# Kernel optimization log

Hardware: AMD Instinct MI355X
Metric: run time of the kernel (lower is better)

Reference implementation:

```python
import jax, jax.numpy as jnp
import numpy as np

B, S, I, H, O, L = 32, 512, 1024, 1024, 1024, 3


def setup_inputs() -> dict:
    key = jax.random.key(0)
    ks = jax.random.split(key, 16)
    sw = 1.0 / np.sqrt(H)  # roughly torch Linear init scale
    inp = {
        "x": jax.random.normal(ks[0], (B, S, I), jnp.float32),
        "h0": jax.random.normal(ks[1], (B, L, H), jnp.float32),
        # gate weights stacked over layers; stored (in, out) so y = x @ W
        "Wx":  jax.random.normal(ks[2], (L, I, H), jnp.float32) * sw,
        "Wz":  jax.random.normal(ks[3], (L, H, H), jnp.float32) * sw,
        "bz":  jax.random.normal(ks[4], (L, H), jnp.float32),   # init.normal_ in original
        "Wr":  jax.random.normal(ks[5], (L, I, H), jnp.float32) * sw,
        "Wh":  jax.random.normal(ks[6], (L, H, H), jnp.float32) * sw,
        "br":  jax.random.normal(ks[7], (L, H), jnp.float32),
        "Wg":  jax.random.normal(ks[8], (L, I, H), jnp.float32) * sw,
        "Whg": jax.random.normal(ks[9], (L, H, H), jnp.float32) * sw,
        "bg":  jax.random.normal(ks[10], (L, H), jnp.float32),
        "Wout": jax.random.normal(ks[11], (H, O), jnp.float32) * sw,
        "bout": jax.random.normal(ks[12], (O,), jnp.float32) * sw,
    }
    return inp


def reference(x, h0, Wx, Wz, bz, Wr, Wh, br, Wg, Whg, bg, Wout, bout):
    n_layers = Wx.shape[0]
    # Original quirk: layer_states only ever gains the LAST layer's ht each
    # timestep; state for layer j at step t is layer_states[t + j]. That is a
    # sliding window of length n_layers over [init states, last-layer hts...].
    window0 = jnp.transpose(h0, (1, 0, 2))  # (L, B, H)

    def step(window, xt):  # window: (L,B,H), xt: (B,I)
        inp = xt
        ht = window[-1]
        for j in range(n_layers):
            s = window[j]
            zt = jax.nn.sigmoid(inp @ Wx[j] + s @ Wz[j] + bz[j])
            rt = jax.nn.sigmoid(inp @ Wr[j] + s @ Wh[j] + br[j])
            ht = zt * s + (1.0 - zt) * jnp.tanh(
                inp @ Wg[j] + (rt * s) @ Whg[j] + bg[j])
            inp = ht  # dropout p=0 is identity
        new_window = jnp.concatenate([window[1:], ht[None]], axis=0)
        y = inp @ Wout + bout
        return new_window, (y, ht)

    _, (ys, hts) = jax.lax.scan(step, window0, jnp.transpose(x, (1, 0, 2)))
    layer_output = jnp.transpose(ys, (1, 0, 2))          # (B, S, O)
    hidden_state = jnp.transpose(hts[-n_layers:], (1, 0, 2))  # (B, L, H)
    return layer_output, hidden_state
```

## Files before the change

### kernel.cpp

```cpp
#include <hip/hip_runtime.h>

#define B_ 32
#define S_ 512
#define H_ 1024
#define L_ 3
#define BH (B_*H_)
#define NBLK 512
#define PLANE 32768

typedef __attribute__((ext_vector_type(8))) short short8;
typedef __attribute__((ext_vector_type(4))) float f4;

__device__ __forceinline__ unsigned short f2bf(float f){
  unsigned int u = __float_as_uint(f);
  u += 0x7fffu + ((u >> 16) & 1u);
  return (unsigned short)(u >> 16);
}
__device__ __forceinline__ float sigmoidf_(float x){
  return 1.0f / (1.0f + __expf(-x));
}
__device__ __forceinline__ int afrag_off(int b, int n){
  int mh = b >> 4, row = b & 15;
  int kb = n >> 5, quad = (n >> 3) & 3, j = n & 7;
  return (((mh * 32 + kb) * 64) + quad * 16 + row) * 8 + j;
}

template<bool DC>
__device__ __forceinline__ short8 ldA(const unsigned short* p){
  short8 v;
  if constexpr (DC)
    asm volatile("global_load_dwordx4 %0, %1, off sc1" : "=&v"(v) : "v"(p));
  else
    asm volatile("global_load_dwordx4 %0, %1, off" : "=&v"(v) : "v"(p));
  return v;
}
template<int N>
__device__ __forceinline__ void waitv(){
  asm volatile("s_waitcnt vmcnt(%0)" :: "i"(N));
  __builtin_amdgcn_sched_barrier(0);
}
__device__ __forceinline__ float ldf_dc(const float* p){
  return __hip_atomic_load(p, __ATOMIC_RELAXED, __HIP_MEMORY_SCOPE_AGENT);
}
__device__ __forceinline__ void stf_dc(float* p, float v){
  __hip_atomic_store(p, v, __ATOMIC_RELAXED, __HIP_MEMORY_SCOPE_AGENT);
}
__device__ __forceinline__ void stu16_dc(unsigned short* p, unsigned short v){
  __hip_atomic_store(p, v, __ATOMIC_RELAXED, __HIP_MEMORY_SCOPE_AGENT);
}

__global__ void prep_WA_packed(const float* __restrict__ Wx, const float* __restrict__ Wz,
                               const float* __restrict__ Wr, const float* __restrict__ Wh,
                               unsigned short* __restrict__ WAp){
  int idx = blockIdx.x * blockDim.x + threadIdx.x;
  int lane = idx & 63;
  int kb = (idx >> 6) & 63;
  int tile = idx >> 12;
  int g = tile >> 7, jt = tile & 127;
  int quad = lane >> 4, l15 = lane & 15;
  int n = jt * 16 + l15;
  int k0 = kb * 32 + quad * 8;
  int col = n & 1023;
  const float* W = (k0 < 1024) ? ((n < 1024) ? Wx : Wr) : ((n < 1024) ? Wz : Wh);
  const float* src = W + ((size_t)g * 1024 + (k0 & 1023)) * 1024 + col;
  short8 v;
  #pragma unroll
  for (int j = 0; j < 8; ++j) v[j] = (short)f2bf(src[(size_t)j * 1024]);
  *(short8*)(WAp + (size_t)idx * 8) = v;
}

__global__ void prep_WB_packed(const float* __restrict__ Wg, const float* __restrict__ Whg,
                               unsigned short* __restrict__ WBp){
  int idx = blockIdx.x * blockDim.x + threadIdx.x;
  int lane = idx & 63;
  int kb = (idx >> 6) & 63;
  int tile = idx >> 12;
  int g = tile >> 6, jt = tile & 63;
  int quad = lane >> 4, l15 = lane & 15;
  int n = jt * 16 + l15;
  int k0 = kb * 32 + quad * 8;
  const float* W = (k0 < 1024) ? Wg : Whg;
  const float* src = W + ((size_t)g * 1024 + (k0 & 1023)) * 1024 + n;
  short8 v;
  #pragma unroll
  for (int j = 0; j < 8; ++j) v[j] = (short)f2bf(src[(size_t)j * 1024]);
  *(short8*)(WBp + (size_t)idx * 8) = v;
}

__global__ void prep_Wout_packed(const float* __restrict__ Wout,
                                 unsigned short* __restrict__ WoutP){
  int idx = blockIdx.x * blockDim.x + threadIdx.x;
  int lane = idx & 63;
  int kb = (idx >> 6) & 31;
  int tile = idx >> 11;
  int quad = lane >> 4, l15 = lane & 15;
  int n = tile * 16 + l15;
  int k0 = kb * 32 + quad * 8;
  const float* src = Wout + (size_t)k0 * 1024 + n;
  short8 v;
  #pragma unroll
  for (int j = 0; j < 8; ++j) v[j] = (short)f2bf(src[(size_t)j * 1024]);
  *(short8*)(WoutP + (size_t)idx * 8) = v;
}

__global__ void prep_X_packed(const float* __restrict__ x, unsigned short* __restrict__ Xp){
  size_t idx = (size_t)blockIdx.x * blockDim.x + threadIdx.x;
  int j = (int)(idx & 7);
  int lane = (int)((idx >> 3) & 63);
  int kb = (int)((idx >> 9) & 31);
  int mh = (int)((idx >> 14) & 1);
  int t = (int)(idx >> 15);
  int b = mh * 16 + (lane & 15);
  int i = kb * 32 + (lane >> 4) * 8 + j;
  Xp[idx] = f2bf(x[((size_t)b * S_ + t) * 1024 + i]);
}

__global__ void prep_H0_kernel(const float* __restrict__ h0,
                               unsigned short* __restrict__ HTb, float* __restrict__ HTf,
                               unsigned short* __restrict__ hfinp){
  int idx = blockIdx.x * blockDim.x + threadIdx.x;
  int h = idx & 1023;
  int b = (idx >> 10) & 31;
  int v = idx >> 15;
  float val = h0[((size_t)b * L_ + v) * 1024 + h];
  HTb[idx] = f2bf(val);
  HTf[idx] = val;
  hfinp[(size_t)v * PLANE + afrag_off(b, h)] = f2bf(val);
}

__device__ __forceinline__ void tree_barrier(unsigned* bar, unsigned target){
  __syncthreads();
  if (threadIdx.x == 0){
    unsigned* sub = bar + (blockIdx.x & 7) * 16;
    unsigned* top = bar + 128;
    unsigned* gen = bar + 144;
    unsigned old = __hip_atomic_fetch_add(sub, 1u, __ATOMIC_RELAXED, __HIP_MEMORY_SCOPE_AGENT);
    if (old == target * (NBLK / 8) - 1u){
      unsigned t2 = __hip_atomic_fetch_add(top, 1u, __ATOMIC_RELAXED, __HIP_MEMORY_SCOPE_AGENT);
      if (t2 == target * 8u - 1u)
        __hip_atomic_store(gen, target, __ATOMIC_RELAXED, __HIP_MEMORY_SCOPE_AGENT);
    }
    while (__hip_atomic_load(gen, __ATOMIC_RELAXED, __HIP_MEMORY_SCOPE_AGENT) < target)
      __builtin_amdgcn_s_sleep(1);
  }
  __syncthreads();
}

template<bool DCI>
__device__ __forceinline__ f4 gemm64_lds(const unsigned short* __restrict__ inp,
                                         const unsigned short* __restrict__ st,
                                         const unsigned short* w,
                                         int mh, int lane){
  const unsigned short* pi = inp + mh * 16384 + lane * 8;
  const unsigned short* ps = st  + mh * 16384 + lane * 8;
  short8 ab[4][8];
  #pragma unroll
  for (int b = 0; b < 4; ++b)
    #pragma unroll
    for (int j = 0; j < 8; ++j)
      ab[b][j] = ldA<DCI>(pi + (size_t)(b * 8 + j) * 512);
  f4 acc = {0.f, 0.f, 0.f, 0.f};
  #pragma unroll
  for (int b = 0; b < 4; ++b){
    short8 wv[8];
    #pragma unroll
    for (int j = 0; j < 8; ++j)
      wv[j] = *(const short8*)(w + (size_t)((b * 8 + j) * 64 + lane) * 8);
    waitv<24>();
    #pragma unroll
    for (int j = 0; j < 8; ++j)
      acc = __builtin_amdgcn_mfma_f32_16x16x32_bf16(ab[b][j], wv[j], acc, 0, 0, 0);
    #pragma unroll
    for (int j = 0; j < 8; ++j)
      ab[b][j] = ldA<true>(ps + (size_t)(b * 8 + j) * 512);
  }
  #pragma unroll
  for (int b = 0; b < 4; ++b){
    short8 wv[8];
    #pragma unroll
    for (int j = 0; j < 8; ++j)
      wv[j] = *(const short8*)(w + (size_t)((32 + b * 8 + j) * 64 + lane) * 8);
    if (b == 0) waitv<24>();
    else if (b == 1) waitv<16>();
    else if (b == 2) waitv<8>();
    else waitv<0>();
    #pragma unroll
    for (int j = 0; j < 8; ++j)
      acc = __builtin_amdgcn_mfma_f32_16x16x32_bf16(ab[b][j], wv[j], acc, 0, 0, 0);
  }
  return acc;
}

__device__ __forceinline__ f4 gemm64_gw(const unsigned short* __restrict__ inp,
                                        const unsigned short* __restrict__ st,
                                        const unsigned short* __restrict__ wg,
                                        int mh, int lane){
  const unsigned short* pi = inp + mh * 16384 + lane * 8;
  const unsigned short* ps = st  + mh * 16384 + lane * 8;
  const unsigned short* pw = wg + lane * 8;
  short8 ab[2][8], wb[2][8];
  #pragma unroll
  for (int b = 0; b < 2; ++b){
    #pragma unroll
    for (int j = 0; j < 8; ++j) ab[b][j] = ldA<true>(pi + (size_t)(b * 8 + j) * 512);
    #pragma unroll
    for (int j = 0; j < 8; ++j) wb[b][j] = ldA<false>(pw + (size_t)(b * 8 + j) * 512);
  }
  f4 acc = {0.f, 0.f, 0.f, 0.f};
  #pragma unroll
  for (int b = 0; b < 8; ++b){
    if (b < 7) waitv<16>(); else waitv<0>();
    #pragma unroll
    for (int j = 0; j < 8; ++j)
      acc = __builtin_amdgcn_mfma_f32_16x16x32_bf16(ab[b & 1][j], wb[b & 1][j], acc, 0, 0, 0);
    if (b < 6){
      const int nb = b + 2;
      #pragma unroll
      for (int j = 0; j < 8; ++j){
        if (nb < 4) ab[b & 1][j] = ldA<true>(pi + (size_t)(nb * 8 + j) * 512);
        else        ab[b & 1][j] = ldA<true>(ps + (size_t)((nb - 4) * 8 + j) * 512);
      }
      #pragma unroll
      for (int j = 0; j < 8; ++j)
        wb[b & 1][j] = ldA<false>(pw + (size_t)(nb * 8 + j) * 512);
    }
  }
  return acc;
}

__global__ __launch_bounds__(128) void gru_persist(
    const unsigned short* __restrict__ WAp, const unsigned short* __restrict__ WBp,
    const unsigned short* __restrict__ Xp,
    unsigned short* __restrict__ hL0p, unsigned short* __restrict__ hL1p,
    unsigned short* __restrict__ hfinp,
    unsigned short* __restrict__ HTb, float* __restrict__ HTf,
    float* __restrict__ zbuf, unsigned short* __restrict__ rsp,
    const float* __restrict__ bz, const float* __restrict__ br,
    const float* __restrict__ bg, unsigned* bar)
{
  __shared__ unsigned short ldsw[32768];
  const int blk = blockIdx.x;
  const int lane = threadIdx.x & 63;
  const int mh = threadIdx.x >> 6;
  const int quad = lane >> 4, l15 = lane & 15;

  {
    const unsigned short* src = (blk < 384) ? WAp + (size_t)blk * 32768
                                            : WBp + (size_t)(blk - 384) * 32768;
    for (int i = threadIdx.x; i < 4096; i += 128)
      *(short8*)(ldsw + (size_t)i * 8) = *(const short8*)(src + (size_t)i * 8);
  }
  __syncthreads();

  const int gA = blk >> 7, jtA = blk & 127;
  int gB = -1, jtB = 0;
  const unsigned short* wBg = nullptr;
  if (blk >= 384){ gB = (blk - 384) >> 6; jtB = (blk - 384) & 63; }
  else if (blk >= 320){ gB = 2; jtB = blk - 320; wBg = WBp + (size_t)(128 + (blk - 320)) * 32768; }

  float biasA = 0.f, biasB = 0.f;
  if (blk < 384){
    int n2 = jtA * 16 + l15;
    biasA = (jtA < 64) ? bz[gA * H_ + n2] : br[gA * H_ + n2 - 1024];
  }
  if (gB >= 0) biasB = bg[gB * H_ + jtB * 16 + l15];

  unsigned tgt = 1;
  for (int s = -4; s <= 2 * S_ - 1; ++s){
    int u = ((s & 1) ? (s - 1) : s) / 2;
    int v = u + 2;
    if (!(s & 1)){
      if (blk < 384){
        int t = u + 2 - gA;
        if (t >= 0 && t < S_){
          int tm = t & 3;
          const unsigned short* inp = (gA == 0) ? Xp + (size_t)t * PLANE
                                    : (gA == 1) ? hL0p + (size_t)tm * PLANE
                                                : hL1p + (size_t)tm * PLANE;
          const unsigned short* st = hfinp + (size_t)(v & 7) * PLANE;
          f4 acc = (gA == 0) ? gemm64_lds<false>(inp, st, ldsw, mh, lane)
                             : gemm64_lds<true >(inp, st, ldsw, mh, lane);
          int n2 = jtA * 16 + l15;
          const float* sf = HTf + (size_t)(v & 7) * BH;
          if (jtA < 64){
            float* zb = zbuf + (size_t)(gA * 4 + tm) * BH;
            #pragma unroll
            for (int r = 0; r < 4; ++r){
              int b = mh * 16 + quad * 4 + r;
              stf_dc(zb + b * H_ + n2, sigmoidf_(acc[r] + biasA));
            }
          } else {
            int n = n2 - 1024;
            unsigned short* rp = rsp + (size_t)(gA * 4 + tm) * PLANE;
            #pragma unroll
            for (int r = 0; r < 4; ++r){
              int b = mh * 16 + quad * 4 + r;
              float sv = ldf_dc(sf + b * H_ + n);
              stu16_dc(rp + afrag_off(b, n), f2bf(sigmoidf_(acc[r] + biasA) * sv));
            }
          }
        }
      }
    } else {
      if (gB >= 0){
        int t = u + 2 - gB;
        if (t >= 0 && t < S_){
          int tm = t & 3;
          const unsigned short* inp = (gB == 0) ? Xp + (size_t)t * PLANE
                                    : (gB == 1) ? hL0p + (size_t)tm * PLANE
                                                : hL1p + (size_t)tm * PLANE;
          const unsigned short* rp = rsp + (size_t)(gB * 4 + tm) * PLANE;
          f4 acc;
          if (wBg)          acc = gemm64_gw(inp, rp, wBg, mh, lane);
          else if (gB == 0) acc = gemm64_lds<false>(inp, rp, ldsw, mh, lane);
          else              acc = gemm64_lds<true >(inp, rp, ldsw, mh, lane);
          int n = jtB * 16 + l15;
          const float* sf = HTf + (size_t)(v & 7) * BH;
          const float* zb = zbuf + (size_t)(gB * 4 + tm) * BH;
          #pragma unroll
          for (int r = 0; r < 4; ++r){
            int b = mh * 16 + quad * 4 + r;
            float gg = tanhf(acc[r] + biasB);
            float z = ldf_dc(zb + b * H_ + n);
            float sv = ldf_dc(sf + b * H_ + n);
            float h = z * sv + (1.f - z) * gg;
            unsigned short hb = f2bf(h);
            if (gB == 2){
              stf_dc(HTf + (size_t)((t + 3) & 7) * BH + b * H_ + n, h);
              HTb[(size_t)(t + 3) * BH + b * H_ + n] = hb;
              stu16_dc(hfinp + (size_t)((t + 3) & 7) * PLANE + afrag_off(b, n), hb);
            } else if (gB == 0){
              stu16_dc(hL0p + (size_t)tm * PLANE + afrag_off(b, n), hb);
            } else {
              stu16_dc(hL1p + (size_t)tm * PLANE + afrag_off(b, n), hb);
            }
          }
        }
      }
    }
    tree_barrier(bar, tgt++);
  }
}

__global__ __launch_bounds__(256) void out_proj_kernel(
    const unsigned short* __restrict__ HTb, const unsigned short* __restrict__ WoutP,
    const float* __restrict__ bout, float* __restrict__ Y){
  int tstep = blockIdx.x >> 2;
  int nblk  = blockIdx.x & 3;
  int wave = threadIdx.x >> 6, lane = threadIdx.x & 63;
  int quad = lane >> 4, l15 = lane & 15;
  const unsigned short* A = HTb + (size_t)(tstep + 3) * BH;
  f4 acc[2][4] = {};
  for (int kk = 0; kk < 32; ++kk){
    int k0 = kk * 32 + quad * 8;
    short8 a0 = *(const short8*)(A + l15 * H_ + k0);
    short8 a1 = *(const short8*)(A + (l15 + 16) * H_ + k0);
    #pragma unroll
    for (int nt = 0; nt < 4; ++nt){
      int tile = nblk * 16 + wave * 4 + nt;
      short8 bv = ((const short8*)WoutP)[((size_t)tile * 32 + kk) * 64 + lane];
      acc[0][nt] = __builtin_amdgcn_mfma_f32_16x16x32_bf16(a0, bv, acc[0][nt], 0, 0, 0);
      acc[1][nt] = __builtin_amdgcn_mfma_f32_16x16x32_bf16(a1, bv, acc[1][nt], 0, 0, 0);
    }
  }
  #pragma unroll
  for (int mt = 0; mt < 2; ++mt)
    #pragma unroll
    for (int nt = 0; nt < 4; ++nt)
      #pragma unroll
      for (int r = 0; r < 4; ++r){
        int b = mt * 16 + quad * 4 + r;
        int n = nblk * 256 + wave * 64 + nt * 16 + l15;
        Y[(size_t)b * (S_ * 1024) + (size_t)tstep * 1024 + n] = acc[mt][nt][r] + bout[n];
      }
}

__global__ void copy_hidden_kernel(const float* __restrict__ HTf, float* __restrict__ out2){
  int idx = blockIdx.x * blockDim.x + threadIdx.x;
  int h = idx & 1023;
  int b = (idx >> 10) & 31;
  int v = idx >> 15;
  out2[((size_t)b * L_ + v) * 1024 + h] = HTf[(size_t)((S_ + v) & 7) * BH + b * H_ + h];
}

extern "C" void kernel_launch(void* const* d_in, const int* in_sizes, int n_in,
                              void* d_out, int out_size, void* d_ws, size_t ws_size,
                              hipStream_t stream){
  (void)in_sizes; (void)n_in; (void)out_size;
  const float* x    = (const float*)d_in[0];
  const float* h0   = (const float*)d_in[1];
  const float* Wx   = (const float*)d_in[2];
  const float* Wz   = (const float*)d_in[3];
  const float* bz   = (const float*)d_in[4];
  const float* Wr   = (const float*)d_in[5];
  const float* Wh   = (const float*)d_in[6];
  const float* br   = (const float*)d_in[7];
  const float* Wg   = (const float*)d_in[8];
  const float* Whg  = (const float*)d_in[9];
  const float* bg   = (const float*)d_in[10];
  const float* Wout = (const float*)d_in[11];
  const float* bout = (const float*)d_in[12];
  float* out = (float*)d_out;

  char* p = (char*)d_ws;
  unsigned short* WAp   = (unsigned short*)p; p += (size_t)384 * 32768 * 2;
  unsigned short* WBp   = (unsigned short*)p; p += (size_t)192 * 32768 * 2;
  unsigned short* WoutP = (unsigned short*)p; p += (size_t)64 * 32 * 64 * 8 * 2;
  unsigned short* Xp    = (unsigned short*)p; p += (size_t)S_ * PLANE * 2;
  unsigned short* HTb   = (unsigned short*)p; p += (size_t)(S_ + 3) * BH * 2;
  float*          HTf   = (float*)p;          p += (size_t)8 * BH * 4;
  unsigned short* hfinp = (unsigned short*)p; p += (size_t)8 * PLANE * 2;
  unsigned short* hL0p  = (unsigned short*)p; p += (size_t)4 * PLANE * 2;
  unsigned short* hL1p  = (unsigned short*)p; p += (size_t)4 * PLANE * 2;
  unsigned short* rsp   = (unsigned short*)p; p += (size_t)12 * PLANE * 2;
  float*          zbuf  = (float*)p;          p += (size_t)12 * BH * 4;
  unsigned*       bar   = (unsigned*)p;       p += 4096;
  if ((size_t)(p - (char*)d_ws) > ws_size) return;

  hipMemsetAsync(bar, 0, 4096, stream);
  prep_WA_packed  <<<6144, 256, 0, stream>>>(Wx, Wz, Wr, Wh, WAp);
  prep_WB_packed  <<<3072, 256, 0, stream>>>(Wg, Whg, WBp);
  prep_Wout_packed<<< 512, 256, 0, stream>>>(Wout, WoutP);
  prep_X_packed   <<<65536, 256, 0, stream>>>(x, Xp);
  prep_H0_kernel  <<<  384, 256, 0, stream>>>(h0, HTb, HTf, hfinp);

  gru_persist<<<NBLK, 128, 0, stream>>>(WAp, WBp, Xp, hL0p, hL1p, hfinp,
                                        HTb, HTf, zbuf, rsp, bz, br, bg, bar);

  out_proj_kernel   <<<2048, 256, 0, stream>>>(HTb, WoutP, bout, out);
  copy_hidden_kernel<<< 384, 256, 0, stream>>>(HTf, out + (size_t)B_ * S_ * 1024);
}
```

Baseline: 7.578 ms.

## Replace global tree barrier with per-timestep dataflow counters between GRU stages

The persistent GRU kernel used to run a lockstep schedule with a grid-wide tree barrier after every half-step. It now gives each stage and layer a counter per timestep. Blocks wait only on the specific producer counters they depend on, including the buffer-reuse hazards, and increment their own counter when done. This removes global barrier latency and lets layers run ahead as a wavefront, at the cost of more atomic polling and subtle dependency logic that could deadlock or race if any dependency is missed.

```diff
diff --git a/kernel.cpp b/kernel.cpp
--- a/kernel.cpp
+++ b/kernel.cpp
@@ -7,6 +7,7 @@
 #define BH (B_*H_)
 #define NBLK 512
 #define PLANE 32768
+#define CNT_BYTES (6*512*32*4)
 
 typedef __attribute__((ext_vector_type(8))) short short8;
 typedef __attribute__((ext_vector_type(4))) float f4;
@@ -47,6 +48,17 @@
 }
 __device__ __forceinline__ void stu16_dc(unsigned short* p, unsigned short v){
   __hip_atomic_store(p, v, __ATOMIC_RELAXED, __HIP_MEMORY_SCOPE_AGENT);
+}
+
+__device__ __forceinline__ unsigned* cptr(unsigned* cnt, int b, int g, int t){
+  return cnt + (size_t)((b * 3 + g) * 512 + t) * 32;
+}
+__device__ __forceinline__ void waitc(unsigned* c, unsigned tgt){
+  while (__hip_atomic_load(c, __ATOMIC_RELAXED, __HIP_MEMORY_SCOPE_AGENT) < tgt)
+    __builtin_amdgcn_s_sleep(1);
+}
+__device__ __forceinline__ void signalc(unsigned* c){
+  __hip_atomic_fetch_add(c, 1u, __ATOMIC_RELAXED, __HIP_MEMORY_SCOPE_AGENT);
 }
 
 __global__ void prep_WA_packed(const float* __restrict__ Wx, const float* __restrict__ Wz,
@@ -128,24 +140,6 @@
   hfinp[(size_t)v * PLANE + afrag_off(b, h)] = f2bf(val);
 }
 
-__device__ __forceinline__ void tree_barrier(unsigned* bar, unsigned target){
-  __syncthreads();
-  if (threadIdx.x == 0){
-    unsigned* sub = bar + (blockIdx.x & 7) * 16;
-    unsigned* top = bar + 128;
-    unsigned* gen = bar + 144;
-    unsigned old = __hip_atomic_fetch_add(sub, 1u, __ATOMIC_RELAXED, __HIP_MEMORY_SCOPE_AGENT);
-    if (old == target * (NBLK / 8) - 1u){
-      unsigned t2 = __hip_atomic_fetch_add(top, 1u, __ATOMIC_RELAXED, __HIP_MEMORY_SCOPE_AGENT);
-      if (t2 == target * 8u - 1u)
-        __hip_atomic_store(gen, target, __ATOMIC_RELAXED, __HIP_MEMORY_SCOPE_AGENT);
-    }
-    while (__hip_atomic_load(gen, __ATOMIC_RELAXED, __HIP_MEMORY_SCOPE_AGENT) < target)
-      __builtin_amdgcn_s_sleep(1);
-  }
-  __syncthreads();
-}
-
 template<bool DCI>
 __device__ __forceinline__ f4 gemm64_lds(const unsigned short* __restrict__ inp,
                                          const unsigned short* __restrict__ st,
@@ -228,6 +222,75 @@
   return acc;
 }
 
+__device__ __forceinline__ void A_body(int gA, int jtA, int mh, int lane, int quad, int l15,
+    int t, const unsigned short* Xp, const unsigned short* hL0p, const unsigned short* hL1p,
+    const unsigned short* hfinp, const float* HTf, float* zbuf, unsigned short* rsp,
+    const unsigned short* ldsw, float biasA){
+  int tm = t & 3, v = t + gA;
+  const unsigned short* inp = (gA == 0) ? Xp + (size_t)t * PLANE
+                            : (gA == 1) ? hL0p + (size_t)tm * PLANE
+                                        : hL1p + (size_t)tm * PLANE;
+  const unsigned short* st = hfinp + (size_t)(v & 7) * PLANE;
+  f4 acc = (gA == 0) ? gemm64_lds<false>(inp, st, ldsw, mh, lane)
+                     : gemm64_lds<true >(inp, st, ldsw, mh, lane);
+  int n2 = jtA * 16 + l15;
+  const float* sf = HTf + (size_t)(v & 7) * BH;
+  if (jtA < 64){
+    float* zb = zbuf + (size_t)(gA * 4 + tm) * BH;
+    #pragma unroll
+    for (int r = 0; r < 4; ++r){
+      int b = mh * 16 + quad * 4 + r;
+      stf_dc(zb + b * H_ + n2, sigmoidf_(acc[r] + biasA));
+    }
+  } else {
+    int n = n2 - 1024;
+    unsigned short* rp = rsp + (size_t)(gA * 4 + tm) * PLANE;
+    #pragma unroll
+    for (int r = 0; r < 4; ++r){
+      int b = mh * 16 + quad * 4 + r;
+      float sv = ldf_dc(sf + b * H_ + n);
+      stu16_dc(rp + afrag_off(b, n), f2bf(sigmoidf_(acc[r] + biasA) * sv));
+    }
+  }
+}
+
+__device__ __forceinline__ void B_body(int gB, int jtB, int mh, int lane, int quad, int l15,
+    int t, const unsigned short* Xp, unsigned short* hL0p, unsigned short* hL1p,
+    unsigned short* hfinp, unsigned short* HTb, float* HTf, const float* zbuf,
+    const unsigned short* rsp, const unsigned short* ldsw, const unsigned short* wBg,
+    float biasB){
+  int tm = t & 3, v = t + gB;
+  const unsigned short* inp = (gB == 0) ? Xp + (size_t)t * PLANE
+                            : (gB == 1) ? hL0p + (size_t)tm * PLANE
+                                        : hL1p + (size_t)tm * PLANE;
+  const unsigned short* rp = rsp + (size_t)(gB * 4 + tm) * PLANE;
+  f4 acc;
+  if (wBg)          acc = gemm64_gw(inp, rp, wBg, mh, lane);
+  else if (gB == 0) acc = gemm64_lds<false>(inp, rp, ldsw, mh, lane);
+  else              acc = gemm64_lds<true >(inp, rp, ldsw, mh, lane);
+  int n = jtB * 16 + l15;
+  const float* sf = HTf + (size_t)(v & 7) * BH;
+  const float* zb = zbuf + (size_t)(gB * 4 + tm) * BH;
+  #pragma unroll
+  for (int r = 0; r < 4; ++r){
+    int b = mh * 16 + quad * 4 + r;
+    float gg = tanhf(acc[r] + biasB);
+    float z = ldf_dc(zb + b * H_ + n);
+    float sv = ldf_dc(sf + b * H_ + n);
+    float h = z * sv + (1.f - z) * gg;
+    unsigned short hb = f2bf(h);
+    if (gB == 2){
+      stf_dc(HTf + (size_t)((t + 3) & 7) * BH + b * H_ + n, h);
+      HTb[(size_t)(t + 3) * BH + b * H_ + n] = hb;
+      stu16_dc(hfinp + (size_t)((t + 3) & 7) * PLANE + afrag_off(b, n), hb);
+    } else if (gB == 0){
+      stu16_dc(hL0p + (size_t)tm * PLANE + afrag_off(b, n), hb);
+    } else {
+      stu16_dc(hL1p + (size_t)tm * PLANE + afrag_off(b, n), hb);
+    }
+  }
+}
+
 __global__ __launch_bounds__(128) void gru_persist(
     const unsigned short* __restrict__ WAp, const unsigned short* __restrict__ WBp,
     const unsigned short* __restrict__ Xp,
@@ -236,7 +299,7 @@
     unsigned short* __restrict__ HTb, float* __restrict__ HTf,
     float* __restrict__ zbuf, unsigned short* __restrict__ rsp,
     const float* __restrict__ bz, const float* __restrict__ br,
-    const float* __restrict__ bg, unsigned* bar)
+    const float* __restrict__ bg, unsigned* cnt)
 {
   __shared__ unsigned short ldsw[32768];
   const int blk = blockIdx.x;
@@ -265,80 +328,64 @@
   }
   if (gB >= 0) biasB = bg[gB * H_ + jtB * 16 + l15];
 
-  unsigned tgt = 1;
-  for (int s = -4; s <= 2 * S_ - 1; ++s){
-    int u = ((s & 1) ? (s - 1) : s) / 2;
-    int v = u + 2;
-    if (!(s & 1)){
-      if (blk < 384){
-        int t = u + 2 - gA;
-        if (t >= 0 && t < S_){
-          int tm = t & 3;
-          const unsigned short* inp = (gA == 0) ? Xp + (size_t)t * PLANE
-                                    : (gA == 1) ? hL0p + (size_t)tm * PLANE
-                                                : hL1p + (size_t)tm * PLANE;
-          const unsigned short* st = hfinp + (size_t)(v & 7) * PLANE;
-          f4 acc = (gA == 0) ? gemm64_lds<false>(inp, st, ldsw, mh, lane)
-                             : gemm64_lds<true >(inp, st, ldsw, mh, lane);
-          int n2 = jtA * 16 + l15;
-          const float* sf = HTf + (size_t)(v & 7) * BH;
-          if (jtA < 64){
-            float* zb = zbuf + (size_t)(gA * 4 + tm) * BH;
-            #pragma unroll
-            for (int r = 0; r < 4; ++r){
-              int b = mh * 16 + quad * 4 + r;
-              stf_dc(zb + b * H_ + n2, sigmoidf_(acc[r] + biasA));
-            }
-          } else {
-            int n = n2 - 1024;
-            unsigned short* rp = rsp + (size_t)(gA * 4 + tm) * PLANE;
-            #pragma unroll
-            for (int r = 0; r < 4; ++r){
-              int b = mh * 16 + quad * 4 + r;
-              float sv = ldf_dc(sf + b * H_ + n);
-              stu16_dc(rp + afrag_off(b, n), f2bf(sigmoidf_(acc[r] + biasA) * sv));
-            }
-          }
+  if (blk < 320){
+    for (int t = 0; t < S_; ++t){
+      if (threadIdx.x == 0){
+        if (gA > 0) waitc(cptr(cnt, 1, gA - 1, t), 64);
+        int w = t + gA - 3;
+        if (w >= 0) waitc(cptr(cnt, 1, 2, w), 64);
+        if (t >= 4) waitc(cptr(cnt, 1, gA, t - 4), 64);
+      }
+      __syncthreads();
+      A_body(gA, jtA, mh, lane, quad, l15, t, Xp, hL0p, hL1p, hfinp, HTf, zbuf, rsp,
+             ldsw, biasA);
+      __syncthreads();
+      if (threadIdx.x == 0) signalc(cptr(cnt, 0, gA, t));
+    }
+  } else if (blk < 384){
+    for (int t = 0; t < S_; ++t){
+      if (threadIdx.x == 0){
+        waitc(cptr(cnt, 1, 1, t), 64);
+        if (t >= 1) waitc(cptr(cnt, 1, 2, t - 1), 64);
+        if (t >= 4) waitc(cptr(cnt, 1, 2, t - 4), 64);
+      }
+      __syncthreads();
+      A_body(2, jtA, mh, lane, quad, l15, t, Xp, hL0p, hL1p, hfinp, HTf, zbuf, rsp,
+             ldsw, biasA);
+      __syncthreads();
+      if (threadIdx.x == 0){
+        signalc(cptr(cnt, 0, 2, t));
+        waitc(cptr(cnt, 0, 2, t), 128);
+        if (t >= 5) waitc(cptr(cnt, 0, 0, t - 5), 128);
+        if (t >= 6) waitc(cptr(cnt, 0, 1, t - 6), 128);
+        if (t >= 7) waitc(cptr(cnt, 0, 2, t - 7), 128);
+        if (t >= 5) waitc(cptr(cnt, 1, 0, t - 5), 64);
+        if (t >= 6) waitc(cptr(cnt, 1, 1, t - 6), 64);
+      }
+      __syncthreads();
+      B_body(2, jtB, mh, lane, quad, l15, t, Xp, hL0p, hL1p, hfinp, HTb, HTf, zbuf, rsp,
+             ldsw, wBg, biasB);
+      __syncthreads();
+      if (threadIdx.x == 0) signalc(cptr(cnt, 1, 2, t));
+    }
+  } else {
+    for (int t = 0; t < S_; ++t){
+      if (threadIdx.x == 0){
+        waitc(cptr(cnt, 0, gB, t), 128);
+        if (gB > 0) waitc(cptr(cnt, 1, gB - 1, t), 64);
+        int w = t + gB - 3;
+        if (w >= 0) waitc(cptr(cnt, 1, 2, w), 64);
+        if (t >= 4){
+          waitc(cptr(cnt, 0, gB + 1, t - 4), 128);
+          waitc(cptr(cnt, 1, gB + 1, t - 4), 64);
         }
       }
-    } else {
-      if (gB >= 0){
-        int t = u + 2 - gB;
-        if (t >= 0 && t < S_){
-          int tm = t & 3;
-          const unsigned short* inp = (gB == 0) ? Xp + (size_t)t * PLANE
-                                    : (gB == 1) ? hL0p + (size_t)tm * PLANE
-                                                : hL1p + (size_t)tm * PLANE;
-          const unsigned short* rp = rsp + (size_t)(gB * 4 + tm) * PLANE;
-          f4 acc;
-          if (wBg)          acc = gemm64_gw(inp, rp, wBg, mh, lane);
-          else if (gB == 0) acc = gemm64_lds<false>(inp, rp, ldsw, mh, lane);
-          else              acc = gemm64_lds<true >(inp, rp, ldsw, mh, lane);
-          int n = jtB * 16 + l15;
-          const float* sf = HTf + (size_t)(v & 7) * BH;
-          const float* zb = zbuf + (size_t)(gB * 4 + tm) * BH;
-          #pragma unroll
-          for (int r = 0; r < 4; ++r){
-            int b = mh * 16 + quad * 4 + r;
-            float gg = tanhf(acc[r] + biasB);
-            float z = ldf_dc(zb + b * H_ + n);
-            float sv = ldf_dc(sf + b * H_ + n);
-            float h = z * sv + (1.f - z) * gg;
-            unsigned short hb = f2bf(h);
-            if (gB == 2){
-              stf_dc(HTf + (size_t)((t + 3) & 7) * BH + b * H_ + n, h);
-              HTb[(size_t)(t + 3) * BH + b * H_ + n] = hb;
-              stu16_dc(hfinp + (size_t)((t + 3) & 7) * PLANE + afrag_off(b, n), hb);
-            } else if (gB == 0){
-              stu16_dc(hL0p + (size_t)tm * PLANE + afrag_off(b, n), hb);
-            } else {
-              stu16_dc(hL1p + (size_t)tm * PLANE + afrag_off(b, n), hb);
-            }
-          }
-        }
-      }
-    }
-    tree_barrier(bar, tgt++);
+      __syncthreads();
+      B_body(gB, jtB, mh, lane, quad, l15, t, Xp, hL0p, hL1p, hfinp, HTb, HTf, zbuf, rsp,
+             ldsw, nullptr, biasB);
+      __syncthreads();
+      if (threadIdx.x == 0) signalc(cptr(cnt, 1, gB, t));
+    }
   }
 }
 
@@ -414,10 +461,10 @@
   unsigned short* hL1p  = (unsigned short*)p; p += (size_t)4 * PLANE * 2;
   unsigned short* rsp   = (unsigned short*)p; p += (size_t)12 * PLANE * 2;
   float*          zbuf  = (float*)p;          p += (size_t)12 * BH * 4;
-  unsigned*       bar   = (unsigned*)p;       p += 4096;
+  unsigned*       cnt   = (unsigned*)p;       p += CNT_BYTES;
   if ((size_t)(p - (char*)d_ws) > ws_size) return;
 
-  hipMemsetAsync(bar, 0, 4096, stream);
+  hipMemsetAsync(cnt, 0, CNT_BYTES, stream);
   prep_WA_packed  <<<6144, 256, 0, stream>>>(Wx, Wz, Wr, Wh, WAp);
   prep_WB_packed  <<<3072, 256, 0, stream>>>(Wg, Whg, WBp);
   prep_Wout_packed<<< 512, 256, 0, stream>>>(Wout, WoutP);
@@ -425,7 +472,7 @@
   prep_H0_kernel  <<<  384, 256, 0, stream>>>(h0, HTb, HTf, hfinp);
 
   gru_persist<<<NBLK, 128, 0, stream>>>(WAp, WBp, Xp, hL0p, hL1p, hfinp,
-                                        HTb, HTf, zbuf, rsp, bz, br, bg, bar);
+                                        HTb, HTf, zbuf, rsp, bz, br, bg, cnt);
 
   out_proj_kernel   <<<2048, 256, 0, stream>>>(HTb, WoutP, bout, out);
   copy_hidden_kernel<<< 384, 256, 0, stream>>>(HTf, out + (size_t)B_ * S_ * 1024);
```

Result: slower. 12.03 ms (+58.7%).

## Split layer-2 candidate GEMM across 128 blocks with split-K LDS reduction

Applied to the files above, without the earlier changes.

Layer-2 candidate-gate work, which streams its weights from global memory, moves off the 64 blocks 320-383 onto blocks 0-127. Each block now handles half the batch for one output tile. Its two waves each do half of K, one wave over the input half and the other over the r*s half, and the partial sums are combined through a small shared buffer before the gate math and state stores. The aim is to shorten the critical path of the global-weight GEMM in the odd phase by spreading it over more blocks. The cost is an extra __syncthreads and each weight tile being read by two blocks.

```diff
diff --git a/kernel.cpp b/kernel.cpp
--- a/kernel.cpp
+++ b/kernel.cpp
@@ -191,38 +191,29 @@
   return acc;
 }
 
-__device__ __forceinline__ f4 gemm64_gw(const unsigned short* __restrict__ inp,
-                                        const unsigned short* __restrict__ st,
-                                        const unsigned short* __restrict__ wg,
-                                        int mh, int lane){
-  const unsigned short* pi = inp + mh * 16384 + lane * 8;
-  const unsigned short* ps = st  + mh * 16384 + lane * 8;
-  const unsigned short* pw = wg + lane * 8;
+__device__ __forceinline__ f4 gemm32_half(const unsigned short* __restrict__ aP,
+                                          const unsigned short* __restrict__ wP){
   short8 ab[2][8], wb[2][8];
   #pragma unroll
   for (int b = 0; b < 2; ++b){
     #pragma unroll
-    for (int j = 0; j < 8; ++j) ab[b][j] = ldA<true>(pi + (size_t)(b * 8 + j) * 512);
-    #pragma unroll
-    for (int j = 0; j < 8; ++j) wb[b][j] = ldA<false>(pw + (size_t)(b * 8 + j) * 512);
+    for (int j = 0; j < 8; ++j) ab[b][j] = ldA<true>(aP + (size_t)(b * 8 + j) * 512);
+    #pragma unroll
+    for (int j = 0; j < 8; ++j) wb[b][j] = ldA<false>(wP + (size_t)(b * 8 + j) * 512);
   }
   f4 acc = {0.f, 0.f, 0.f, 0.f};
   #pragma unroll
-  for (int b = 0; b < 8; ++b){
-    if (b < 7) waitv<16>(); else waitv<0>();
+  for (int b = 0; b < 4; ++b){
+    if (b < 3) waitv<16>(); else waitv<0>();
     #pragma unroll
     for (int j = 0; j < 8; ++j)
       acc = __builtin_amdgcn_mfma_f32_16x16x32_bf16(ab[b & 1][j], wb[b & 1][j], acc, 0, 0, 0);
-    if (b < 6){
+    if (b < 2){
       const int nb = b + 2;
       #pragma unroll
-      for (int j = 0; j < 8; ++j){
-        if (nb < 4) ab[b & 1][j] = ldA<true>(pi + (size_t)(nb * 8 + j) * 512);
-        else        ab[b & 1][j] = ldA<true>(ps + (size_t)((nb - 4) * 8 + j) * 512);
-      }
+      for (int j = 0; j < 8; ++j) ab[b & 1][j] = ldA<true>(aP + (size_t)(nb * 8 + j) * 512);
       #pragma unroll
-      for (int j = 0; j < 8; ++j)
-        wb[b & 1][j] = ldA<false>(pw + (size_t)(nb * 8 + j) * 512);
+      for (int j = 0; j < 8; ++j) wb[b & 1][j] = ldA<false>(wP + (size_t)(nb * 8 + j) * 512);
     }
   }
   return acc;
@@ -239,6 +230,7 @@
     const float* __restrict__ bg, unsigned* bar)
 {
   __shared__ unsigned short ldsw[32768];
+  __shared__ f4 part[64];
   const int blk = blockIdx.x;
   const int lane = threadIdx.x & 63;
   const int mh = threadIdx.x >> 6;
@@ -254,16 +246,19 @@
 
   const int gA = blk >> 7, jtA = blk & 127;
   int gB = -1, jtB = 0;
-  const unsigned short* wBg = nullptr;
   if (blk >= 384){ gB = (blk - 384) >> 6; jtB = (blk - 384) & 63; }
-  else if (blk >= 320){ gB = 2; jtB = blk - 320; wBg = WBp + (size_t)(128 + (blk - 320)) * 32768; }
-
-  float biasA = 0.f, biasB = 0.f;
+
+  const bool isB2 = blk < 128;
+  const int jt2 = blk & 63, bh2 = (blk >> 6) & 1;
+  const unsigned short* w2 = WBp + (size_t)(128 + jt2) * 32768;
+
+  float biasA = 0.f, biasB = 0.f, bias2 = 0.f;
   if (blk < 384){
     int n2 = jtA * 16 + l15;
     biasA = (jtA < 64) ? bz[gA * H_ + n2] : br[gA * H_ + n2 - 1024];
   }
   if (gB >= 0) biasB = bg[gB * H_ + jtB * 16 + l15];
+  if (isB2)   bias2 = bg[2 * H_ + jt2 * 16 + l15];
 
   unsigned tgt = 1;
   for (int s = -4; s <= 2 * S_ - 1; ++s){
@@ -307,13 +302,10 @@
         if (t >= 0 && t < S_){
           int tm = t & 3;
           const unsigned short* inp = (gB == 0) ? Xp + (size_t)t * PLANE
-                                    : (gB == 1) ? hL0p + (size_t)tm * PLANE
-                                                : hL1p + (size_t)tm * PLANE;
+                                                : hL0p + (size_t)tm * PLANE;
           const unsigned short* rp = rsp + (size_t)(gB * 4 + tm) * PLANE;
-          f4 acc;
-          if (wBg)          acc = gemm64_gw(inp, rp, wBg, mh, lane);
-          else if (gB == 0) acc = gemm64_lds<false>(inp, rp, ldsw, mh, lane);
-          else              acc = gemm64_lds<true >(inp, rp, ldsw, mh, lane);
+          f4 acc = (gB == 0) ? gemm64_lds<false>(inp, rp, ldsw, mh, lane)
+                             : gemm64_lds<true >(inp, rp, ldsw, mh, lane);
           int n = jtB * 16 + l15;
           const float* sf = HTf + (size_t)(v & 7) * BH;
           const float* zb = zbuf + (size_t)(gB * 4 + tm) * BH;
@@ -325,14 +317,39 @@
             float sv = ldf_dc(sf + b * H_ + n);
             float h = z * sv + (1.f - z) * gg;
             unsigned short hb = f2bf(h);
-            if (gB == 2){
+            if (gB == 0) stu16_dc(hL0p + (size_t)tm * PLANE + afrag_off(b, n), hb);
+            else         stu16_dc(hL1p + (size_t)tm * PLANE + afrag_off(b, n), hb);
+          }
+        }
+      } else if (isB2){
+        int t = u;
+        if (t >= 0 && t < S_){
+          int tm = t & 3;
+          const unsigned short* aPlane = (mh == 0) ? hL1p + (size_t)tm * PLANE
+                                                   : rsp + (size_t)(8 + tm) * PLANE;
+          const unsigned short* aP = aPlane + bh2 * 16384 + lane * 8;
+          const unsigned short* wP = w2 + mh * 16384 + lane * 8;
+          f4 acc = gemm32_half(aP, wP);
+          if (mh == 1) part[lane] = acc;
+          __syncthreads();
+          if (mh == 0){
+            f4 p2 = part[lane];
+            #pragma unroll
+            for (int i = 0; i < 4; ++i) acc[i] += p2[i];
+            int n = jt2 * 16 + l15;
+            const float* sf = HTf + (size_t)((t + 2) & 7) * BH;
+            const float* zb = zbuf + (size_t)(8 + tm) * BH;
+            #pragma unroll
+            for (int r = 0; r < 4; ++r){
+              int b = bh2 * 16 + quad * 4 + r;
+              float gg = tanhf(acc[r] + bias2);
+              float z = ldf_dc(zb + b * H_ + n);
+              float sv = ldf_dc(sf + b * H_ + n);
+              float h = z * sv + (1.f - z) * gg;
+              unsigned short hb = f2bf(h);
               stf_dc(HTf + (size_t)((t + 3) & 7) * BH + b * H_ + n, h);
               HTb[(size_t)(t + 3) * BH + b * H_ + n] = hb;
               stu16_dc(hfinp + (size_t)((t + 3) & 7) * PLANE + afrag_off(b, n), hb);
-            } else if (gB == 0){
-              stu16_dc(hL0p + (size_t)tm * PLANE + afrag_off(b, n), hb);
-            } else {
-              stu16_dc(hL1p + (size_t)tm * PLANE + afrag_off(b, n), hb);
             }
           }
         }
```

After: 7.225 ms. 1.05x faster.
